# Optimization experiments

Hardware: AMD Instinct MI355X
Metric: run time of the kernel (lower is better)

Reference implementation:

```python
import jax, jax.numpy as jnp
import numpy as np

B, T1, T2, D = 16, 64, 64, 1024
PROJ = D // 2


def setup_inputs() -> dict:
    key = jax.random.key(0)
    k1, k2, k3 = jax.random.split(key, 3)
    x = jax.random.normal(k1, (B, T1, T2, D), dtype=jnp.float32)
    # glorot-style scale for params
    W_proj = jax.random.normal(k2, (D, PROJ), dtype=jnp.float32) * (2.0 / (D + PROJ)) ** 0.5
    v_score = jax.random.normal(k3, (PROJ,), dtype=jnp.float32) * (1.0 / PROJ) ** 0.5
    return {"x": x, "W_proj": W_proj, "v_score": v_score}


def reference(x, W_proj, v_score):
    # proj_input = tanh(tensordot(x, W_proj, axes=(3,0)))  -> (B, T1, T2, PROJ)
    proj = jnp.tanh(jnp.einsum('btsd,dp->btsp', x, W_proj))
    # att_scores = tensordot(proj, v_score, axes=(3,0))    -> (B, T1, T2)
    scores = jnp.einsum('btsp,p->bts', proj, v_score)
    # softmax over last axis (T2), weighted sum of x over T2 -> (B, T1, D)
    attn = jax.nn.softmax(scores, axis=-1)
    out = jnp.einsum('bts,btsd->btd', attn, x)
    return out
```

## Files before the change

### kernel.cpp

```cpp
#include <hip/hip_runtime.h>
#include <hip/hip_bf16.h>
#include <math.h>

#define B_    16
#define T1_   64
#define T2_   64
#define D_    1024
#define PROJ_ 512
#define BM    64
#define NKH   16
#define HALFK 512

typedef __attribute__((ext_vector_type(8))) short bf16x8;
typedef __attribute__((ext_vector_type(4))) float f32x4;
typedef __attribute__((ext_vector_type(4))) unsigned int u32x4;

__device__ __forceinline__ unsigned short f2bf(float f) {
  unsigned int u = __builtin_bit_cast(unsigned int, f);
  u += 0x7FFFu + ((u >> 16) & 1u);
  return (unsigned short)(u >> 16);
}

__device__ __forceinline__ float fast_tanh(float a) {
  float t = __builtin_amdgcn_exp2f(a * 2.885390081777927f);
  return 1.0f - 2.0f * __builtin_amdgcn_rcpf(t + 1.0f);
}

__global__ __launch_bounds__(256) void make_bfrag(
    const float* __restrict__ W, unsigned short* __restrict__ wt) {
  __shared__ float tile[32][33];
  const int t  = blockIdx.x;
  const int np = blockIdx.y;
  const int tx = threadIdx.x & 31;
  const int ty = threadIdx.x >> 5;
#pragma unroll
  for (int i = 0; i < 4; ++i)
    tile[ty + i * 8][tx] =
        W[(size_t)(t * 32 + ty + i * 8) * PROJ_ + np * 32 + tx];
  __syncthreads();
  if (threadIdx.x < 128) {
    const int sub  = threadIdx.x >> 6;
    const int lane = threadIdx.x & 63;
    const int llo = lane & 15, lhi = lane >> 4;
    unsigned short o[8];
#pragma unroll
    for (int j = 0; j < 8; ++j)
      o[j] = f2bf(tile[lhi * 8 + j][sub * 16 + llo]);
    const int n16 = np * 2 + sub;
    *(u32x4*)(wt + ((size_t)(t * 32 + n16) * 64 + lane) * 8) = *(const u32x4*)o;
  }
}

__global__ __launch_bounds__(512, 4) void fused_kernel(
    const float* __restrict__ x, const unsigned short* __restrict__ wt,
    const float* __restrict__ v, float* __restrict__ out) {
  __shared__ __align__(16) char smem[65536];
  float (*sp)[9] = (float(*)[9])smem;
  float* attn    = (float*)(smem + 2304);
  f32x4* xred    = (f32x4*)(smem + 2560);

  const int tid  = threadIdx.x;
  const int lane = tid & 63;
  const int wid  = tid >> 6;
  const int llo  = lane & 15, lhi = lane >> 4;
  const int swz  = (llo & 7) << 4;
  const int bt   = blockIdx.x;
  const int m0   = bt * BM;

  f32x4 acc[4][4];
#pragma unroll
  for (int mf = 0; mf < 4; ++mf)
#pragma unroll
    for (int nf = 0; nf < 4; ++nf) acc[mf][nf] = (f32x4){0.f, 0.f, 0.f, 0.f};

  const u32x4* wt4 = (const u32x4*)wt;
  const int bbase = (wid * 4) * 64 + lane;

  u32x4 rb[4];
#pragma unroll
  for (int nf = 0; nf < 4; ++nf) rb[nf] = wt4[bbase + nf * 64];

#define STAGE(H)                                                              \
  {                                                                           \
    _Pragma("unroll")                                                         \
    for (int r = 0; r < 8; ++r) {                                             \
      const int p = r * 512 + tid;                                            \
      const int row = p >> 6, pc = p & 63;                                    \
      const float* s = x + (size_t)(m0 + row) * D_ + (H) * HALFK + pc * 8;    \
      float4 a = *(const float4*)s;                                           \
      float4 b = *(const float4*)(s + 4);                                     \
      unsigned short o[8] = {f2bf(a.x), f2bf(a.y), f2bf(a.z), f2bf(a.w),      \
                             f2bf(b.x), f2bf(b.y), f2bf(b.z), f2bf(b.w)};     \
      const int db = (row * 1024 + pc * 16) ^ ((row & 7) << 4);               \
      *(u32x4*)(smem + db) = *(const u32x4*)o;                                \
    }                                                                         \
  }

#define KLOOP(H)                                                              \
  {                                                                           \
    _Pragma("unroll 2")                                                       \
    for (int ks = 0; ks < NKH; ++ks) {                                        \
      const int t32 = (H) * NKH + ks;                                         \
      const int kb = ks * 64 + lhi * 16;                                      \
      bf16x8 af0 = *(const bf16x8*)(smem + ((( 0 + llo) * 1024 + kb) ^ swz)); \
      bf16x8 af1 = *(const bf16x8*)(smem + (((16 + llo) * 1024 + kb) ^ swz)); \
      bf16x8 af2 = *(const bf16x8*)(smem + (((32 + llo) * 1024 + kb) ^ swz)); \
      bf16x8 af3 = *(const bf16x8*)(smem + (((48 + llo) * 1024 + kb) ^ swz)); \
      u32x4 rbn[4];                                                           \
      if (t32 + 1 < 32) {                                                     \
        _Pragma("unroll")                                                     \
        for (int nf = 0; nf < 4; ++nf)                                        \
          rbn[nf] = wt4[(size_t)(t32 + 1) * 2048 + bbase + nf * 64];          \
      }                                                                       \
      __builtin_amdgcn_s_setprio(1);                                          \
      _Pragma("unroll")                                                       \
      for (int nf = 0; nf < 4; ++nf) {                                        \
        bf16x8 bfr = *(const bf16x8*)&rb[nf];                                 \
        acc[0][nf] = __builtin_amdgcn_mfma_f32_16x16x32_bf16(af0, bfr, acc[0][nf], 0, 0, 0); \
        acc[1][nf] = __builtin_amdgcn_mfma_f32_16x16x32_bf16(af1, bfr, acc[1][nf], 0, 0, 0); \
        acc[2][nf] = __builtin_amdgcn_mfma_f32_16x16x32_bf16(af2, bfr, acc[2][nf], 0, 0, 0); \
        acc[3][nf] = __builtin_amdgcn_mfma_f32_16x16x32_bf16(af3, bfr, acc[3][nf], 0, 0, 0); \
      }                                                                       \
      __builtin_amdgcn_s_setprio(0);                                          \
      if (t32 + 1 < 32) {                                                     \
        _Pragma("unroll")                                                     \
        for (int nf = 0; nf < 4; ++nf) rb[nf] = rbn[nf];                      \
      }                                                                       \
    }                                                                         \
  }

  STAGE(0)
  __syncthreads();
  KLOOP(0)
  __syncthreads();
  STAGE(1)
  __syncthreads();
  KLOOP(1)
  __syncthreads();
#undef STAGE
#undef KLOOP

  {
    const float vv0 = v[wid * 64 +  0 + llo];
    const float vv1 = v[wid * 64 + 16 + llo];
    const float vv2 = v[wid * 64 + 32 + llo];
    const float vv3 = v[wid * 64 + 48 + llo];
#pragma unroll
    for (int mf = 0; mf < 4; ++mf) {
      float pr[4] = {0.f, 0.f, 0.f, 0.f};
#pragma unroll
      for (int r = 0; r < 4; ++r) {
        pr[r] += fast_tanh(acc[mf][0][r]) * vv0;
        pr[r] += fast_tanh(acc[mf][1][r]) * vv1;
        pr[r] += fast_tanh(acc[mf][2][r]) * vv2;
        pr[r] += fast_tanh(acc[mf][3][r]) * vv3;
      }
#pragma unroll
      for (int r = 0; r < 4; ++r) {
        float p = pr[r];
        p += __shfl_xor(p, 1, 64);
        p += __shfl_xor(p, 2, 64);
        p += __shfl_xor(p, 4, 64);
        p += __shfl_xor(p, 8, 64);
        if (llo == 0) sp[mf * 16 + lhi * 4 + r][wid] = p;
      }
    }
  }
  __syncthreads();

  if (tid < BM) {
    float s = 0.f;
#pragma unroll
    for (int w = 0; w < 8; ++w) s += sp[tid][w];
    float mx = s;
#pragma unroll
    for (int mask = 1; mask < 64; mask <<= 1)
      mx = fmaxf(mx, __shfl_xor(mx, mask, 64));
    const float e = __builtin_amdgcn_exp2f((s - mx) * 1.442695040888963f);
    float sum = e;
#pragma unroll
    for (int mask = 1; mask < 64; mask <<= 1)
      sum += __shfl_xor(sum, mask, 64);
    attn[tid] = e * __builtin_amdgcn_rcpf(sum);
  }
  __syncthreads();

  const int c4 = tid & 255;
  const int sh = tid >> 8;
  const float* xg = x + ((size_t)m0 + sh * 32) * D_ + c4 * 4;
  f32x4 o0 = {0.f,0.f,0.f,0.f}, o1 = o0, o2 = o0, o3 = o0;
#pragma unroll
  for (int s = 0; s < 32; s += 4) {
    const float w0 = attn[sh * 32 + s + 0];
    const float w1 = attn[sh * 32 + s + 1];
    const float w2 = attn[sh * 32 + s + 2];
    const float w3 = attn[sh * 32 + s + 3];
    const float4 a0 = *(const float4*)(xg + (size_t)(s + 0) * D_);
    const float4 a1 = *(const float4*)(xg + (size_t)(s + 1) * D_);
    const float4 a2 = *(const float4*)(xg + (size_t)(s + 2) * D_);
    const float4 a3 = *(const float4*)(xg + (size_t)(s + 3) * D_);
    o0[0] += w0 * a0.x; o0[1] += w0 * a0.y; o0[2] += w0 * a0.z; o0[3] += w0 * a0.w;
    o1[0] += w1 * a1.x; o1[1] += w1 * a1.y; o1[2] += w1 * a1.z; o1[3] += w1 * a1.w;
    o2[0] += w2 * a2.x; o2[1] += w2 * a2.y; o2[2] += w2 * a2.z; o2[3] += w2 * a2.w;
    o3[0] += w3 * a3.x; o3[1] += w3 * a3.y; o3[2] += w3 * a3.z; o3[3] += w3 * a3.w;
  }
  f32x4 o;
#pragma unroll
  for (int j = 0; j < 4; ++j) o[j] = (o0[j] + o1[j]) + (o2[j] + o3[j]);
  if (sh == 1) xred[c4] = o;
  __syncthreads();
  if (sh == 0) {
    f32x4 o2b = xred[c4];
    float4 res = {o[0] + o2b[0], o[1] + o2b[1], o[2] + o2b[2], o[3] + o2b[3]};
    *(float4*)(out + (size_t)bt * D_ + c4 * 4) = res;
  }
}

extern "C" void kernel_launch(void* const* d_in, const int* in_sizes, int n_in,
                              void* d_out, int out_size, void* d_ws, size_t ws_size,
                              hipStream_t stream) {
  const float* x = (const float*)d_in[0];
  const float* W = (const float*)d_in[1];
  const float* v = (const float*)d_in[2];
  float* out = (float*)d_out;
  unsigned short* Wt = (unsigned short*)d_ws;

  make_bfrag<<<dim3(32, PROJ_ / 32), 256, 0, stream>>>(W, Wt);
  fused_kernel<<<B_ * T1_, 512, 0, stream>>>(x, Wt, v, out);
}
```

Baseline: 128.9 us.

## Split fused kernel into scores kernel and separate weighted-sum kernel

Splits the fused kernel in two. The first kernel computes the attention softmax weights and writes them to workspace; a new second kernel re-reads x and computes the weighted sum. It also stops buffering the next B fragment in separate registers (loads now go straight into rb inside the MFMA loop) and lowers the staging unroll. This may cut register pressure and raise occupancy in the GEMM kernel, at the cost of an extra launch and a second full read of x from global memory or L2.

```diff
diff --git a/kernel.cpp b/kernel.cpp
--- a/kernel.cpp
+++ b/kernel.cpp
@@ -51,13 +51,11 @@
   }
 }
 
-__global__ __launch_bounds__(512, 4) void fused_kernel(
+__global__ __launch_bounds__(512, 4) void scores_kernel(
     const float* __restrict__ x, const unsigned short* __restrict__ wt,
-    const float* __restrict__ v, float* __restrict__ out) {
+    const float* __restrict__ v, float* __restrict__ attnws) {
   __shared__ __align__(16) char smem[65536];
   float (*sp)[9] = (float(*)[9])smem;
-  float* attn    = (float*)(smem + 2304);
-  f32x4* xred    = (f32x4*)(smem + 2560);
 
   const int tid  = threadIdx.x;
   const int lane = tid & 63;
@@ -82,7 +80,7 @@
 
 #define STAGE(H)                                                              \
   {                                                                           \
-    _Pragma("unroll")                                                         \
+    _Pragma("unroll 2")                                                       \
     for (int r = 0; r < 8; ++r) {                                             \
       const int p = r * 512 + tid;                                            \
       const int row = p >> 6, pc = p & 63;                                    \
@@ -106,12 +104,6 @@
       bf16x8 af1 = *(const bf16x8*)(smem + (((16 + llo) * 1024 + kb) ^ swz)); \
       bf16x8 af2 = *(const bf16x8*)(smem + (((32 + llo) * 1024 + kb) ^ swz)); \
       bf16x8 af3 = *(const bf16x8*)(smem + (((48 + llo) * 1024 + kb) ^ swz)); \
-      u32x4 rbn[4];                                                           \
-      if (t32 + 1 < 32) {                                                     \
-        _Pragma("unroll")                                                     \
-        for (int nf = 0; nf < 4; ++nf)                                        \
-          rbn[nf] = wt4[(size_t)(t32 + 1) * 2048 + bbase + nf * 64];          \
-      }                                                                       \
       __builtin_amdgcn_s_setprio(1);                                          \
       _Pragma("unroll")                                                       \
       for (int nf = 0; nf < 4; ++nf) {                                        \
@@ -120,12 +112,10 @@
         acc[1][nf] = __builtin_amdgcn_mfma_f32_16x16x32_bf16(af1, bfr, acc[1][nf], 0, 0, 0); \
         acc[2][nf] = __builtin_amdgcn_mfma_f32_16x16x32_bf16(af2, bfr, acc[2][nf], 0, 0, 0); \
         acc[3][nf] = __builtin_amdgcn_mfma_f32_16x16x32_bf16(af3, bfr, acc[3][nf], 0, 0, 0); \
+        if (t32 + 1 < 32)                                                     \
+          rb[nf] = wt4[(size_t)(t32 + 1) * 2048 + bbase + nf * 64];           \
       }                                                                       \
       __builtin_amdgcn_s_setprio(0);                                          \
-      if (t32 + 1 < 32) {                                                     \
-        _Pragma("unroll")                                                     \
-        for (int nf = 0; nf < 4; ++nf) rb[nf] = rbn[nf];                      \
-      }                                                                       \
     }                                                                         \
   }
 
@@ -181,20 +171,27 @@
 #pragma unroll
     for (int mask = 1; mask < 64; mask <<= 1)
       sum += __shfl_xor(sum, mask, 64);
-    attn[tid] = e * __builtin_amdgcn_rcpf(sum);
-  }
-  __syncthreads();
-
-  const int c4 = tid & 255;
-  const int sh = tid >> 8;
-  const float* xg = x + ((size_t)m0 + sh * 32) * D_ + c4 * 4;
+    attnws[bt * BM + tid] = e * __builtin_amdgcn_rcpf(sum);
+  }
+}
+
+__global__ __launch_bounds__(256) void out_kernel(
+    const float* __restrict__ x, const float* __restrict__ attnws,
+    float* __restrict__ out) {
+  const int bt  = blockIdx.x;
+  const int tid = threadIdx.x;
+  __shared__ float attn[T2_];
+  if (tid < T2_) attn[tid] = attnws[bt * T2_ + tid];
+  __syncthreads();
+
+  const float* xg = x + (size_t)bt * (T2_ * D_) + tid * 4;
   f32x4 o0 = {0.f,0.f,0.f,0.f}, o1 = o0, o2 = o0, o3 = o0;
-#pragma unroll
-  for (int s = 0; s < 32; s += 4) {
-    const float w0 = attn[sh * 32 + s + 0];
-    const float w1 = attn[sh * 32 + s + 1];
-    const float w2 = attn[sh * 32 + s + 2];
-    const float w3 = attn[sh * 32 + s + 3];
+#pragma unroll 4
+  for (int s = 0; s < T2_; s += 4) {
+    const float w0 = attn[s + 0];
+    const float w1 = attn[s + 1];
+    const float w2 = attn[s + 2];
+    const float w3 = attn[s + 3];
     const float4 a0 = *(const float4*)(xg + (size_t)(s + 0) * D_);
     const float4 a1 = *(const float4*)(xg + (size_t)(s + 1) * D_);
     const float4 a2 = *(const float4*)(xg + (size_t)(s + 2) * D_);
@@ -204,16 +201,11 @@
     o2[0] += w2 * a2.x; o2[1] += w2 * a2.y; o2[2] += w2 * a2.z; o2[3] += w2 * a2.w;
     o3[0] += w3 * a3.x; o3[1] += w3 * a3.y; o3[2] += w3 * a3.z; o3[3] += w3 * a3.w;
   }
-  f32x4 o;
-#pragma unroll
-  for (int j = 0; j < 4; ++j) o[j] = (o0[j] + o1[j]) + (o2[j] + o3[j]);
-  if (sh == 1) xred[c4] = o;
-  __syncthreads();
-  if (sh == 0) {
-    f32x4 o2b = xred[c4];
-    float4 res = {o[0] + o2b[0], o[1] + o2b[1], o[2] + o2b[2], o[3] + o2b[3]};
-    *(float4*)(out + (size_t)bt * D_ + c4 * 4) = res;
-  }
+  float4 res = {(o0[0] + o1[0]) + (o2[0] + o3[0]),
+                (o0[1] + o1[1]) + (o2[1] + o3[1]),
+                (o0[2] + o1[2]) + (o2[2] + o3[2]),
+                (o0[3] + o1[3]) + (o2[3] + o3[3])};
+  *(float4*)(out + (size_t)bt * D_ + tid * 4) = res;
 }
 
 extern "C" void kernel_launch(void* const* d_in, const int* in_sizes, int n_in,
@@ -224,7 +216,9 @@
   const float* v = (const float*)d_in[2];
   float* out = (float*)d_out;
   unsigned short* Wt = (unsigned short*)d_ws;
+  float* attnws = (float*)((char*)d_ws + (1 << 20));
 
   make_bfrag<<<dim3(32, PROJ_ / 32), 256, 0, stream>>>(W, Wt);
-  fused_kernel<<<B_ * T1_, 512, 0, stream>>>(x, Wt, v, out);
-}
+  scores_kernel<<<B_ * T1_, 512, 0, stream>>>(x, Wt, v, attnws);
+  out_kernel<<<B_ * T1_, 256, 0, stream>>>(x, attnws, out);
+}
```

After: 133.2 us. 1.03x slower.
